# Optimization experiments

Measured on AMD Instinct MI355X. Metric: run time of the kernel, lower is better.

Reference implementation:

```python
import jax
import jax.numpy as jnp
from jax import lax
import numpy as np

BETA = 0.5
IPOT_ITERS = 50
IPOT_K = 1
EPS = 1e-5  # F.normalize eps


def _l2_normalize(x, eps=EPS):
    n = jnp.linalg.norm(x, axis=-1, keepdims=True)
    return x / jnp.maximum(n, eps)


def cost_matrix_cosine(x, y):
    # x: [b, m, d], y: [b, n, d] -> 1 - cosine_sim : [b, m, n]
    return 1.0 - jnp.einsum('bmd,bnd->bmn', _l2_normalize(x), _l2_normalize(y))


def ipot(C, x_len, x_pad, y_len, y_pad, joint_pad, beta, iteration, k):
    # C: [b, m, n] (txt x img). Mirrors UNITER's ipot (no_grad).
    b, m, n = C.shape
    jp_T = jnp.swapaxes(joint_pad, 1, 2)                      # [b, n, m]
    A = jnp.where(jp_T, 0.0, jnp.exp(-jnp.swapaxes(C, 1, 2) / beta))  # [b, n, m]
    T0 = jnp.where(jp_T, 0.0, jnp.ones((b, n, m), C.dtype))
    sigma0 = jnp.where(x_pad, 0.0, 1.0 / x_len[:, None])      # [b, m]
    xl = x_len[:, None, None]
    yl = y_len[:, None, None]
    x_mask = (x_pad.astype(C.dtype) * 1e4)[:, None, :]        # [b, 1, m]
    y_mask = (y_pad.astype(C.dtype) * 1e4)[:, None, :]        # [b, 1, n]

    def outer(carry, _):
        T, sigma = carry
        Q = A * T                                             # [b, n, m]
        def inner(sig, _):
            # sig: [b, m]
            qs = jnp.einsum('bnm,bm->bn', Q, sig)[:, None, :]  # [b, 1, n]
            delta = 1.0 / (yl * qs + y_mask)                   # [b, 1, n]
            sig_new = 1.0 / (xl * jnp.matmul(delta, Q) + x_mask)  # [b, 1, m]
            return sig_new[:, 0, :], delta
        sigma, deltas = lax.scan(inner, sigma, None, length=k)
        delta = deltas[-1]                                     # [b, 1, n]
        T = delta[:, 0, :, None] * Q * sigma[:, None, :]       # [b, n, m]
        return (T, sigma), None

    (T, _), _ = lax.scan(outer, (T0, sigma0), None, length=iteration)
    return jnp.where(jp_T, 0.0, T)


def optimal_transport_dist(txt_emb, img_emb, txt_pad, img_pad,
                           beta=BETA, iteration=IPOT_ITERS, k=IPOT_K):
    cost = cost_matrix_cosine(txt_emb, img_emb)               # [b, tl, il]
    joint_pad = txt_pad[:, :, None] | img_pad[:, None, :]
    cost = jnp.where(joint_pad, 0.0, cost)
    txt_len = (txt_pad.shape[1] - jnp.sum(txt_pad, axis=1)).astype(cost.dtype)
    img_len = (img_pad.shape[1] - jnp.sum(img_pad, axis=1)).astype(cost.dtype)
    T = ipot(lax.stop_gradient(cost), txt_len, txt_pad, img_len, img_pad,
             joint_pad, beta, iteration, k)                   # [b, il, tl]
    T = lax.stop_gradient(T)
    # trace(cost @ T) without materializing [b, tl, tl]
    return jnp.einsum('bmn,bnm->b', cost, T)


def setup_inputs() -> dict:
    key = jax.random.key(0)
    ks = jax.random.split(key, 6)
    B, TL, IL, D = 256, 128, 100, 768
    sequence_output = jax.random.normal(ks[0], (B, TL + IL, D), dtype=jnp.float32)
    input_ids = jax.random.randint(ks[1], (B, TL), 0, 30522)
    image_feat = jax.random.normal(ks[2], (B, IL, D), dtype=jnp.float32)
    # realistic padding: valid prefix of random length, padded suffix
    txt_len = jax.random.randint(ks[3], (B,), TL // 2, TL + 1)
    img_len = jax.random.randint(ks[4], (B,), IL // 2, IL + 1)
    txt_pad = jnp.arange(TL)[None, :] >= txt_len[:, None]
    img_pad = jnp.arange(IL)[None, :] >= img_len[:, None]
    is_correct = jax.random.randint(ks[5], (B,), 0, 2)
    return {
        'sequence_output': sequence_output,
        'input_ids': input_ids,
        'image_feat': image_feat,
        'txt_pad': txt_pad,
        'img_pad': img_pad,
        'is_correct': is_correct,
    }


def reference(sequence_output, input_ids, image_feat, txt_pad, img_pad, is_correct):
    tl = input_ids.shape[1]
    il = image_feat.shape[1]
    txt_emb = sequence_output[:, :tl, :].astype(jnp.float32)
    img_emb = sequence_output[:, tl:tl + il, :].astype(jnp.float32)
    ot_dist = optimal_transport_dist(txt_emb, img_emb, txt_pad, img_pad)
    ot_dist = ot_dist.astype(sequence_output.dtype)
    pos = is_correct == 1
    neg = is_correct == 0
    pos_sum = jnp.sum(jnp.where(pos, ot_dist, 0.0))
    neg_sum = jnp.sum(jnp.where(neg, ot_dist, 0.0))
    denom = jnp.sum(pos) + jnp.sum(neg)
    ot_loss = (pos_sum - neg_sum) / denom.astype(ot_dist.dtype)
    return ot_loss


if __name__ == '__main__':
    out = reference(**setup_inputs())
    print(out)
```

## Files before the change

### kernel.cpp

```cpp
#include <hip/hip_runtime.h>
#include <math.h>
#include <stdint.h>

#define TL 128
#define IL 100
#define NP 112
#define DIM 768
#define NSEQ 228
#define KT 32
#define NT 1024
#define NWAVE 16
#define ITERS 50

typedef float f32x4 __attribute__((ext_vector_type(4)));
typedef short short8 __attribute__((ext_vector_type(8)));

__device__ __forceinline__ uint16_t f2bf(float x) {
    union { float f; uint32_t u; } v; v.f = x;
    uint32_t r = v.u + 0x7FFFu + ((v.u >> 16) & 1u);
    return (uint16_t)(r >> 16);
}
__device__ __forceinline__ float bf2f(uint16_t h) {
    union { float f; uint32_t u; } v; v.u = ((uint32_t)h) << 16;
    return v.f;
}

__device__ __forceinline__ float xorsum64(float x) {
    x += __shfl_xor(x, 1);
    x += __shfl_xor(x, 2);
    x += __shfl_xor(x, 4);
    x += __shfl_xor(x, 8);
    x += __shfl_xor(x, 16);
    x += __shfl_xor(x, 32);
    return x;
}

__device__ __forceinline__ void gemm_barrier() {
    __builtin_amdgcn_sched_barrier(0);
    asm volatile("s_waitcnt lgkmcnt(0)" ::: "memory");
    __builtin_amdgcn_s_barrier();
    __builtin_amdgcn_sched_barrier(0);
}

#define CONVERT_STORE(vv, par) do {                                            \
    uint16_t* base_ = &u.stg[par][0];                                          \
    _Pragma("unroll")                                                          \
    for (int r = 0; r < 2; r++) if (act[r]) {                                  \
        float4 x = vv[r];                                                      \
        nrm[r] += x.x*x.x + x.y*x.y + x.z*x.z + x.w*x.w;                       \
        uint16_t h0 = f2bf(x.x), h1 = f2bf(x.y), h2 = f2bf(x.z), h3 = f2bf(x.w); \
        uint16_t l0 = f2bf(x.x - bf2f(h0)), l1 = f2bf(x.y - bf2f(h1));         \
        uint16_t l2 = f2bf(x.z - bf2f(h2)), l3 = f2bf(x.w - bf2f(h3));         \
        uint64_t hq  = (uint64_t)h0 | ((uint64_t)h1<<16) | ((uint64_t)h2<<32) | ((uint64_t)h3<<48); \
        uint64_t lq8 = (uint64_t)l0 | ((uint64_t)l1<<16) | ((uint64_t)l2<<32) | ((uint64_t)l3<<48); \
        *(uint64_t*)(base_ + off_hi[r])        = hq;                           \
        *(uint64_t*)(base_ + (off_hi[r] ^ 32)) = lq8;                          \
    }                                                                          \
} while (0)

#define PREFETCH(vv, cidx) do {                                                \
    _Pragma("unroll")                                                          \
    for (int r = 0; r < 2; r++) if (act[r])                                    \
        vv[r] = *(const float4*)(gp[r] + (cidx) * KT);                         \
} while (0)

#define MFMA_CHUNK(par) do {                                                   \
    const uint16_t* base_ = &u.stg[par][0];                                    \
    short8 ah, al, bh[4], bl[4];                                               \
    {                                                                          \
        int m = 16 * wm + lr;                                                  \
        int s = (lq + m + (m >> 3)) & 7;                                       \
        int ao = m * 64 + 8 * s;                                               \
        ah = *(const short8*)(base_ + ao);                                     \
        al = *(const short8*)(base_ + (ao ^ 32));                              \
    }                                                                          \
    _Pragma("unroll")                                                          \
    for (int q = 0; q < 4; q++) if (q < NQ) {                                  \
        int n  = 16 * (4*wn + q) + lr;                                         \
        int rr = TL + n;                                                       \
        int s  = (lq + rr + (rr >> 3)) & 7;                                    \
        int bo = rr * 64 + 8 * s;                                              \
        bh[q] = *(const short8*)(base_ + bo);                                  \
        bl[q] = *(const short8*)(base_ + (bo ^ 32));                           \
    }                                                                          \
    _Pragma("unroll")                                                          \
    for (int q = 0; q < 4; q++) if (q < NQ) {                                  \
        acc[q] = __builtin_amdgcn_mfma_f32_16x16x32_bf16(ah, bh[q], acc[q], 0, 0, 0); \
        acc[q] = __builtin_amdgcn_mfma_f32_16x16x32_bf16(ah, bl[q], acc[q], 0, 0, 0); \
        acc[q] = __builtin_amdgcn_mfma_f32_16x16x32_bf16(al, bh[q], acc[q], 0, 0, 0); \
    }                                                                          \
} while (0)

__global__ void __launch_bounds__(NT, 4)
WRA_ot_kernel(const float* __restrict__ seq,
              const int* __restrict__ txt_pad,
              const int* __restrict__ img_pad,
              const int* __restrict__ is_correct,
              float* __restrict__ out, int nblocks)
{
    __shared__ __align__(16) union {
        uint16_t stg[2][240 * 64];
        float As[896 * 16];
        struct {
            float pq[NP * 32];
            float ps[TL * 33];
            float dlv[TL];
        } ip;
    } u;
    __shared__ __align__(16) float sums[NSEQ];
    __shared__ __align__(16) float xm[TL];
    __shared__ __align__(16) float ym[NP];
    __shared__ __align__(16) float inx[TL];
    __shared__ __align__(16) float iny[NP];
    __shared__ __align__(16) float sgf[TL];
    __shared__ float red[NWAVE];
    __shared__ int cnt[2];

    const int t    = threadIdx.x;
    const int b    = blockIdx.x;
    const int w    = t >> 6;
    const int lane = t & 63;

    if (t < 2) cnt[t] = 0;
    if (t < NSEQ) sums[t] = 0.0f;
    __syncthreads();
    if (t < TL) {
        int p = txt_pad[b * TL + t] ? 1 : 0;
        xm[t] = p ? 1e4f : 0.0f;
        if (p) atomicAdd(&cnt[0], 1);
    } else if (t < TL + IL) {
        int p = img_pad[b * IL + (t - TL)] ? 1 : 0;
        ym[t - TL] = p ? 1e4f : 0.0f;
        if (p) atomicAdd(&cnt[1], 1);
    } else if (t < TL + NP) {
        ym[t - TL] = 1e4f;
    }

    const float* Xg = seq + (size_t)b * NSEQ * DIM;
    const float* Yg = Xg + (size_t)TL * DIM;

    const float* gp[2];
    int   off_hi[2];
    int   srow[2];
    bool  act[2];
    float nrm[2];
#pragma unroll
    for (int r = 0; r < 2; r++) {
        int f = t + NT * r;
        act[r] = (f < 1824);
        nrm[r] = 0.0f;
        int f2 = act[r] ? f : 0;
        bool isX = (f2 < 1024);
        int row = isX ? (f2 >> 3) : ((f2 - 1024) >> 3);
        int kc  = (f2 & 7) << 2;
        gp[r] = (isX ? Xg : Yg) + row * DIM + kc;
        int rr = isX ? row : (TL + row);
        srow[r] = rr;
        int q = (f2 & 7) >> 1;
        int h = f2 & 1;
        int s = (q + rr + (rr >> 3)) & 7;
        off_hi[r] = rr * 64 + 8 * s + 4 * h;
    }
    {
        uint32_t* s32 = (uint32_t*)&u.stg[0][0];
        for (int i = t; i < 384 * 2; i += NT) {
            int par = (i < 384) ? 0 : 1;
            int off = i - par * 384;
            s32[par * 7680 + 228 * 32 + off] = 0;
        }
    }

    const int wm = w >> 1;
    const int wn = w & 1;
    const int NQ = wn ? 3 : 4;
    f32x4 acc[4];
#pragma unroll
    for (int q = 0; q < 4; q++) acc[q] = (f32x4){0.f, 0.f, 0.f, 0.f};

    const int lr = lane & 15, lq = lane >> 4;

    float4 va[2], vb[2];
    PREFETCH(va, 0);
    PREFETCH(vb, 1);
    CONVERT_STORE(va, 0);
    PREFETCH(va, 2);
    gemm_barrier();

#pragma unroll 1
    for (int cc = 0; cc < 24; cc += 2) {
        {
            if (cc < 23) {
                CONVERT_STORE(vb, 1);
                if (cc < 21) PREFETCH(vb, cc + 3);
            }
            MFMA_CHUNK(0);
            gemm_barrier();
        }
        {
            if (cc + 1 < 23) {
                CONVERT_STORE(va, 0);
                if (cc + 1 < 21) PREFETCH(va, cc + 4);
            }
            MFMA_CHUNK(1);
            gemm_barrier();
        }
    }

#pragma unroll
    for (int r = 0; r < 2; r++) if (act[r]) atomicAdd(&sums[srow[r]], nrm[r]);
#pragma unroll
    for (int q = 0; q < 4; q++) if (q < NQ)
#pragma unroll
        for (int rg = 0; rg < 4; rg++) {
            int m = 16 * wm + 4*lq + rg;
            int n = 16 * (4*wn + q) + lr;
            int mi_ = m >> 2, ni_ = n >> 2;
            int word = ((mi_ + (ni_ << 5)) << 4)
                     + (((n & 3) ^ ((mi_ >> 1) & 3)) << 2) + (m & 3);
            u.As[word] = acc[q][rg];
        }
    __syncthreads();
    if (t < TL)            inx[t]      = 1.0f / fmaxf(sqrtf(sums[t]), 1e-5f);
    else if (t < NSEQ)     iny[t - TL] = 1.0f / fmaxf(sqrtf(sums[t]), 1e-5f);
    else if (t < TL + NP)  iny[t - TL] = 1.0f;
    __syncthreads();

    const float xlen = (float)(TL - cnt[0]);
    const float ylen = (float)(IL - cnt[1]);
    const int mI = t & 31;
    const int nI = t >> 5;
    const bool activeN = (nI < 28);

    float rx[4], xmv[4], ry[4], ymv[4];
    {
        float4 a0 = *(const float4*)&inx[4*mI];
        rx[0]=a0.x; rx[1]=a0.y; rx[2]=a0.z; rx[3]=a0.w;
        float4 b0 = *(const float4*)&xm[4*mI];
        xmv[0]=b0.x; xmv[1]=b0.y; xmv[2]=b0.z; xmv[3]=b0.w;
        if (activeN) {
            float4 c0 = *(const float4*)&iny[4*nI];
            ry[0]=c0.x; ry[1]=c0.y; ry[2]=c0.z; ry[3]=c0.w;
            float4 d0 = *(const float4*)&ym[4*nI];
            ymv[0]=d0.x; ymv[1]=d0.y; ymv[2]=d0.z; ymv[3]=d0.w;
        } else {
#pragma unroll
            for (int j = 0; j < 4; j++) { ry[j] = 1.0f; ymv[j] = 1e4f; }
        }
    }

    float aa[4][4], qq[4][4];
    if (activeN) {
#pragma unroll
        for (int j = 0; j < 4; j++) {
            float4 d0 = *(const float4*)&u.As[(t << 4) + ((j ^ ((mI >> 1) & 3)) << 2)];
            float dv[4] = {d0.x, d0.y, d0.z, d0.w};
#pragma unroll
            for (int i = 0; i < 4; i++) {
                bool pad = (xmv[i] > 0.0f) || (ymv[j] > 0.0f);
                float cc = pad ? 0.0f : (1.0f - dv[i] * rx[i] * ry[j]);
                float av = pad ? 0.0f : expf(-2.0f * cc);
                aa[j][i] = av; qq[j][i] = av;
            }
        }
    } else {
#pragma unroll
        for (int j = 0; j < 4; j++)
#pragma unroll
            for (int i = 0; i < 4; i++) { aa[j][i] = 0.0f; qq[j][i] = 0.0f; }
    }
    __syncthreads();

    float sg[4];
#pragma unroll
    for (int i = 0; i < 4; i++) sg[i] = (xmv[i] > 0.0f) ? 0.0f : (1.0f / xlen);

    float dl[4];
    for (int it = 0; it < ITERS; ++it) {
        if (activeN) {
#pragma unroll
            for (int j = 0; j < 4; j++) {
                float pj = qq[j][0]*sg[0] + qq[j][1]*sg[1] + qq[j][2]*sg[2] + qq[j][3]*sg[3];
                int n = 4*nI + j;
                u.ip.pq[(n << 5) + (mI ^ (n & 31))] = pj;
            }
        }
        __syncthreads();
        if (t < NP) {
            const float* row = &u.ip.pq[t << 5];
            const int nb = t & 31;
            float s0 = 0.f, s1 = 0.f, s2 = 0.f, s3 = 0.f;
#pragma unroll
            for (int k = 0; k < 32; k += 4) {
                s0 += row[(k+0) ^ nb];
                s1 += row[(k+1) ^ nb];
                s2 += row[(k+2) ^ nb];
                s3 += row[(k+3) ^ nb];
            }
            float qs = (s0 + s1) + (s2 + s3);
            u.ip.dlv[t] = __builtin_amdgcn_rcpf(ylen * qs + ym[t]);
        }
        __syncthreads();
        if (activeN) {
            float4 dv = *(const float4*)&u.ip.dlv[4 * nI];
            dl[0]=dv.x; dl[1]=dv.y; dl[2]=dv.z; dl[3]=dv.w;
#pragma unroll
            for (int i = 0; i < 4; i++) {
                float s = dl[0]*qq[0][i] + dl[1]*qq[1][i] + dl[2]*qq[2][i] + dl[3]*qq[3][i];
                u.ip.ps[(4*mI + i) * 33 + nI] = s;
            }
        } else {
            dl[0]=dl[1]=dl[2]=dl[3]=0.0f;
        }
        __syncthreads();
        if (t < TL) {
            const float* row = &u.ip.ps[t * 33];
            float s0 = 0.f, s1 = 0.f, s2 = 0.f, s3 = 0.f;
#pragma unroll
            for (int k = 0; k < 28; k += 4) {
                s0 += row[k+0]; s1 += row[k+1]; s2 += row[k+2]; s3 += row[k+3];
            }
            sgf[t] = __builtin_amdgcn_rcpf(xlen * ((s0+s1)+(s2+s3)) + xm[t]);
        }
        __syncthreads();
        {
            float4 sv = *(const float4*)&sgf[4 * mI];
            sg[0]=sv.x; sg[1]=sv.y; sg[2]=sv.z; sg[3]=sv.w;
        }
        if (it < ITERS - 1) {
#pragma unroll
            for (int j = 0; j < 4; j++) {
                float dj = dl[j];
#pragma unroll
                for (int i = 0; i < 4; i++)
                    qq[j][i] = (qq[j][i] * aa[j][i]) * (dj * sg[i]);
            }
        }
    }

    float local = 0.0f;
#pragma unroll
    for (int j = 0; j < 4; j++)
#pragma unroll
        for (int i = 0; i < 4; i++) {
            float av = aa[j][i];
            float cc = (av > 0.0f) ? (-0.5f * logf(av)) : 0.0f;
            local += cc * qq[j][i] * (dl[j] * sg[i]);
        }
    local = xorsum64(local);
    if (lane == 0) red[w] = local;
    __syncthreads();
    if (t == 0) {
        float tot = 0.0f;
#pragma unroll
        for (int k = 0; k < NWAVE; k++) tot += red[k];
        float sgn = (is_correct[b] == 1) ? 1.0f : -1.0f;
        atomicAdd(out, sgn * tot / (float)nblocks);
    }
}

extern "C" void kernel_launch(void* const* d_in, const int* in_sizes, int n_in,
                              void* d_out, int out_size, void* d_ws, size_t ws_size,
                              hipStream_t stream) {
    const float* seq   = (const float*)d_in[0];
    const int* txt_pad = (const int*)d_in[3];
    const int* img_pad = (const int*)d_in[4];
    const int* is_corr = (const int*)d_in[5];
    float* out = (float*)d_out;
    const int B = in_sizes[5];

    hipMemsetAsync(out, 0, sizeof(float), stream);
    WRA_ot_kernel<<<B, NT, 0, stream>>>(seq, txt_pad, img_pad, is_corr, out, B);
}
```

Measured before the change: 353.7 us.

## Split IPOT row reductions across four lanes and remap m ownership to strided layout

Each row reduction in the iterative IPOT loop (over 32 partial sums for delta, 28 for sigma) is now split across four threads, each summing a contiguous slice, then combined with two xor-shuffles. This shortens the serial critical path between barriers in all 50 iterations. To support this, each thread's m elements change from contiguous (4*mI+i) to strided (mI+32*i). The cosine-matrix shared-memory layout, its swizzle, and the padded strides of the partial-sum buffers change to match. The risk is different bank-conflict patterns and more active threads per reduction phase.

```diff
diff --git a/kernel.cpp b/kernel.cpp
--- a/kernel.cpp
+++ b/kernel.cpp
@@ -102,8 +102,8 @@
         uint16_t stg[2][240 * 64];
         float As[896 * 16];
         struct {
-            float pq[NP * 32];
-            float ps[TL * 33];
+            float pq[NP * 33];
+            float ps[TL * 29];
             float dlv[TL];
         } ip;
     } u;
@@ -214,9 +214,8 @@
         for (int rg = 0; rg < 4; rg++) {
             int m = 16 * wm + 4*lq + rg;
             int n = 16 * (4*wn + q) + lr;
-            int mi_ = m >> 2, ni_ = n >> 2;
-            int word = ((mi_ + (ni_ << 5)) << 4)
-                     + (((n & 3) ^ ((mi_ >> 1) & 3)) << 2) + (m & 3);
+            int tp = (m & 31) + ((n >> 2) << 5);
+            int word = (tp << 4) + (((n & 3) ^ (tp & 3)) << 2) + (m >> 5);
             u.As[word] = acc[q][rg];
         }
     __syncthreads();
@@ -233,10 +232,11 @@
 
     float rx[4], xmv[4], ry[4], ymv[4];
     {
-        float4 a0 = *(const float4*)&inx[4*mI];
-        rx[0]=a0.x; rx[1]=a0.y; rx[2]=a0.z; rx[3]=a0.w;
-        float4 b0 = *(const float4*)&xm[4*mI];
-        xmv[0]=b0.x; xmv[1]=b0.y; xmv[2]=b0.z; xmv[3]=b0.w;
+#pragma unroll
+        for (int i = 0; i < 4; i++) {
+            rx[i]  = inx[mI + 32*i];
+            xmv[i] = xm[mI + 32*i];
+        }
         if (activeN) {
             float4 c0 = *(const float4*)&iny[4*nI];
             ry[0]=c0.x; ry[1]=c0.y; ry[2]=c0.z; ry[3]=c0.w;
@@ -252,7 +252,7 @@
     if (activeN) {
 #pragma unroll
         for (int j = 0; j < 4; j++) {
-            float4 d0 = *(const float4*)&u.As[(t << 4) + ((j ^ ((mI >> 1) & 3)) << 2)];
+            float4 d0 = *(const float4*)&u.As[(t << 4) + ((j ^ (t & 3)) << 2)];
             float dv[4] = {d0.x, d0.y, d0.z, d0.w};
 #pragma unroll
             for (int i = 0; i < 4; i++) {
@@ -280,24 +280,18 @@
 #pragma unroll
             for (int j = 0; j < 4; j++) {
                 float pj = qq[j][0]*sg[0] + qq[j][1]*sg[1] + qq[j][2]*sg[2] + qq[j][3]*sg[3];
-                int n = 4*nI + j;
-                u.ip.pq[(n << 5) + (mI ^ (n & 31))] = pj;
+                u.ip.pq[(4*nI + j) * 33 + mI] = pj;
             }
         }
         __syncthreads();
-        if (t < NP) {
-            const float* row = &u.ip.pq[t << 5];
-            const int nb = t & 31;
-            float s0 = 0.f, s1 = 0.f, s2 = 0.f, s3 = 0.f;
-#pragma unroll
-            for (int k = 0; k < 32; k += 4) {
-                s0 += row[(k+0) ^ nb];
-                s1 += row[(k+1) ^ nb];
-                s2 += row[(k+2) ^ nb];
-                s3 += row[(k+3) ^ nb];
-            }
-            float qs = (s0 + s1) + (s2 + s3);
-            u.ip.dlv[t] = __builtin_amdgcn_rcpf(ylen * qs + ym[t]);
+        if (t < 4 * NP) {
+            int n = t >> 2, qh = t & 3;
+            const float* row = &u.ip.pq[n * 33 + 8 * qh];
+            float s = ((row[0] + row[1]) + (row[2] + row[3]))
+                    + ((row[4] + row[5]) + (row[6] + row[7]));
+            s += __shfl_xor(s, 1);
+            s += __shfl_xor(s, 2);
+            if (qh == 0) u.ip.dlv[n] = __builtin_amdgcn_rcpf(ylen * s + ym[n]);
         }
         __syncthreads();
         if (activeN) {
@@ -306,26 +300,26 @@
 #pragma unroll
             for (int i = 0; i < 4; i++) {
                 float s = dl[0]*qq[0][i] + dl[1]*qq[1][i] + dl[2]*qq[2][i] + dl[3]*qq[3][i];
-                u.ip.ps[(4*mI + i) * 33 + nI] = s;
+                u.ip.ps[(mI + 32*i) * 29 + nI] = s;
             }
         } else {
             dl[0]=dl[1]=dl[2]=dl[3]=0.0f;
         }
         __syncthreads();
-        if (t < TL) {
-            const float* row = &u.ip.ps[t * 33];
-            float s0 = 0.f, s1 = 0.f, s2 = 0.f, s3 = 0.f;
-#pragma unroll
-            for (int k = 0; k < 28; k += 4) {
-                s0 += row[k+0]; s1 += row[k+1]; s2 += row[k+2]; s3 += row[k+3];
-            }
-            sgf[t] = __builtin_amdgcn_rcpf(xlen * ((s0+s1)+(s2+s3)) + xm[t]);
+        if (t < 4 * TL) {
+            int m = t >> 2, qh = t & 3;
+            const float* row = &u.ip.ps[m * 29 + 7 * qh];
+            float s = ((row[0] + row[1]) + (row[2] + row[3]))
+                    + ((row[4] + row[5]) + row[6]);
+            s += __shfl_xor(s, 1);
+            s += __shfl_xor(s, 2);
+            if (qh == 0) sgf[m] = __builtin_amdgcn_rcpf(xlen * s + xm[m]);
         }
         __syncthreads();
-        {
-            float4 sv = *(const float4*)&sgf[4 * mI];
-            sg[0]=sv.x; sg[1]=sv.y; sg[2]=sv.z; sg[3]=sv.w;
-        }
+        sg[0] = sgf[mI];
+        sg[1] = sgf[mI + 32];
+        sg[2] = sgf[mI + 64];
+        sg[3] = sgf[mI + 96];
         if (it < ITERS - 1) {
 #pragma unroll
             for (int j = 0; j < 4; j++) {
```

Measured after the change: 356.5 us. No clear change (+0.8%).
